# Performance work log

Hardware: AMD Instinct MI355X
Metric: run time of the kernel (lower is better)

Reference implementation:

```python
import jax, jax.numpy as jnp
import numpy as np

HIDDEN = 1024
HEADS = 16
HEAD = HIDDEN // HEADS
EXPAND = 4096
EPS = 1e-5


def layer_norm(x, g, b):
    mu = jnp.mean(x, axis=-1, keepdims=True)
    var = jnp.mean((x - mu) ** 2, axis=-1, keepdims=True)
    return (x - mu) * jax.lax.rsqrt(var + EPS) * g + b


def setup_inputs() -> dict:
    key = jax.random.key(0)
    ks = jax.random.split(key, 12)
    s = 0.02
    return {
        "x": jax.random.normal(ks[0], (4, 2048, HIDDEN), dtype=jnp.float32),
        "Wqkv": jax.random.normal(ks[1], (HIDDEN, 3 * HIDDEN), dtype=jnp.float32) * s,
        "bqkv": jnp.zeros((3 * HIDDEN,), jnp.float32),
        "Wproj": jax.random.normal(ks[2], (HIDDEN, HIDDEN), dtype=jnp.float32) * s,
        "bproj": jnp.zeros((HIDDEN,), jnp.float32),
        "W1": jax.random.normal(ks[3], (HIDDEN, EXPAND), dtype=jnp.float32) * s,
        "b1": jnp.zeros((EXPAND,), jnp.float32),
        "W2": jax.random.normal(ks[4], (EXPAND, HIDDEN), dtype=jnp.float32) * s,
        "b2": jnp.zeros((HIDDEN,), jnp.float32),
        "g1": jnp.ones((HIDDEN,), jnp.float32),
        "be1": jnp.zeros((HIDDEN,), jnp.float32),
        "g2": jnp.ones((HIDDEN,), jnp.float32),
        "be2": jnp.zeros((HIDDEN,), jnp.float32),
    }


def attention(x, Wqkv, bqkv, Wproj, bproj):
    B, L, _ = x.shape
    qkv = (x @ Wqkv + bqkv).reshape(B, L, 3, HEADS, HEAD)
    q, k, v = [qkv[:, :, i].transpose(0, 2, 1, 3) for i in range(3)]  # [B,H,L,D]
    attn = jnp.einsum("bnld,bnkd->bnlk", q, k) / np.sqrt(HEAD).astype(np.float32)
    attn = jax.nn.softmax(attn, axis=-1)
    o = jnp.einsum("bnlk,bnkd->bnld", attn, v)
    o = o.transpose(0, 2, 1, 3).reshape(B, L, HIDDEN)
    return o @ Wproj + bproj


def reference(x, Wqkv, bqkv, Wproj, bproj, W1, b1, W2, b2, g1, be1, g2, be2):
    # post-norm transformer block (pre_norm=False), dropout=0 (eval)
    h = layer_norm(x + attention(x, Wqkv, bqkv, Wproj, bproj), g1, be1)
    ff = jax.nn.gelu(h @ W1 + b1, approximate=False) @ W2 + b2
    return layer_norm(h + ff, g2, be2)
```

## Files before the change

kernel.cpp:

```cpp
#include <hip/hip_runtime.h>
#include <hip/hip_bf16.h>
#include <math.h>


typedef __bf16 bf16_t;
typedef __bf16 bf16x8 __attribute__((ext_vector_type(8)));
typedef __bf16 bf16x4 __attribute__((ext_vector_type(4)));
typedef float f32x4 __attribute__((ext_vector_type(4)));
typedef float f32x16 __attribute__((ext_vector_type(16)));

#define HID   1024
#define NHEAD 16
#define HD    64
#define EXPD  4096
#define LSEQ  2048
#define BATCH 4
#define MROWS (BATCH * LSEQ)

#if __has_builtin(__builtin_amdgcn_exp2f)
#define EXP2F __builtin_amdgcn_exp2f
#else
#define EXP2F exp2f
#endif

__device__ __forceinline__ void gld_lds16(const bf16_t* g, bf16_t* l) {
  __builtin_amdgcn_global_load_lds(
      (const __attribute__((address_space(1))) void*)g,
      (__attribute__((address_space(3))) void*)l, 16, 0, 0);
}

__device__ __forceinline__ void vmwait(int n) {
  if (n == 8)      asm volatile("s_waitcnt vmcnt(8)" ::: "memory");
  else if (n == 4) asm volatile("s_waitcnt vmcnt(4)" ::: "memory");
  else if (n == 3) asm volatile("s_waitcnt vmcnt(3)" ::: "memory");
  else if (n == 0) asm volatile("s_waitcnt vmcnt(0)" ::: "memory");
}

__device__ __forceinline__ void block_bar() {
  asm volatile("" ::: "memory");
  __builtin_amdgcn_s_barrier();
  asm volatile("" ::: "memory");
}

__device__ __forceinline__ void swap32(unsigned& a, unsigned& b) {
#if __has_builtin(__builtin_amdgcn_permlane32_swap)
  auto r = __builtin_amdgcn_permlane32_swap(a, b, false, false);
  a = r[0]; b = r[1];
#else
  bool hiL = ((threadIdx.x & 63) >= 32);
  unsigned pa = (unsigned)__shfl_xor((int)a, 32, 64);
  unsigned pb = (unsigned)__shfl_xor((int)b, 32, 64);
  unsigned na = hiL ? pb : a;
  unsigned nb = hiL ? b : pa;
  a = na; b = nb;
#endif
}

__device__ __forceinline__ unsigned pk_bf16(float lo, float hi) {
  bf16_t l = (bf16_t)lo, h = (bf16_t)hi;
  unsigned short ul, uh;
  __builtin_memcpy(&ul, &l, 2);
  __builtin_memcpy(&uh, &h, 2);
  return (unsigned)ul | ((unsigned)uh << 16);
}

__device__ __forceinline__ float gelu_t(float v) {
  float u = v * (0.7978845608028654f + 0.0356774081f * v * v);
  float e = EXP2F(u * 2.885390082f);
  float th = (e - 1.f) / (e + 1.f);
  return 0.5f * v * (1.f + th);
}

__global__ __launch_bounds__(256) void cvt_bf16(const float* __restrict__ in,
                                                bf16_t* __restrict__ out, int n4) {
  int i = blockIdx.x * 256 + threadIdx.x;
  if (i >= n4) return;
  float4 v = ((const float4*)in)[i];
  bf16x4 o;
  o[0] = (bf16_t)v.x; o[1] = (bf16_t)v.y; o[2] = (bf16_t)v.z; o[3] = (bf16_t)v.w;
  ((bf16x4*)out)[i] = o;
}

__global__ __launch_bounds__(256) void transpose_cvt(const float* __restrict__ W,
                                                     bf16_t* __restrict__ Wt,
                                                     int K, int N) {
  __shared__ float tile[32][33];
  int n0 = blockIdx.x * 32, k0 = blockIdx.y * 32;
  int tx = threadIdx.x & 31, ty = threadIdx.x >> 5;
#pragma unroll
  for (int i = 0; i < 32; i += 8)
    tile[ty + i][tx] = W[(size_t)(k0 + ty + i) * N + n0 + tx];
  __syncthreads();
#pragma unroll
  for (int i = 0; i < 32; i += 8)
    Wt[(size_t)(n0 + ty + i) * K + k0 + tx] = (bf16_t)tile[tx][ty + i];
}

template <int BM, int BN, int NTHR>
__global__ __launch_bounds__(NTHR, (NTHR == 512 ? 4 : 3))
void gemm_k(const bf16_t* __restrict__ A,
            const bf16_t* __restrict__ Bt,
            const float* __restrict__ bias,
            void* __restrict__ C,
            float* __restrict__ C2,
            bf16_t* __restrict__ vTo,
            int M, int N, int K, int mode) {
  constexpr int WC = (NTHR / 64) / 2;
  constexpr int AL = BM * 4 / NTHR;
  constexpr int BL = BN * 4 / NTHR;
  constexpr int LOADS = AL + BL;
  constexpr int RSTEP = NTHR >> 2;
  __shared__ bf16_t smem[3 * BM * 32 + 3 * BN * 32];
  bf16_t* As = smem;
  bf16_t* Bs = smem + 3 * BM * 32;

  const int nbx = gridDim.x;
  int p = blockIdx.y * nbx + blockIdx.x;
  const int GM = 8;
  int group = p / (GM * nbx);
  int idx = p - group * (GM * nbx);
  const int by = group * GM + (idx & (GM - 1));
  const int bx = idx >> 3;
  const int n0 = bx * BN, m0 = by * BM;

  const int zz = blockIdx.z;
  const int kLen = K / (int)gridDim.z;
  const int kOff = zz * kLen;

  const int t = threadIdx.x;
  const int lane = t & 63, w = t >> 6;
  const int wr = w / WC, wc = w % WC;
  const int quad = lane >> 4, l16 = lane & 15;

  f32x4 acc[4][4];
#pragma unroll
  for (int i = 0; i < 4; ++i)
#pragma unroll
    for (int j = 0; j < 4; ++j) acc[i][j] = (f32x4){0.f, 0.f, 0.f, 0.f};

  const int r0 = t >> 2;
  const unsigned ksw = (((unsigned)t & 3u) ^ ((unsigned)(r0 >> 1) & 3u)) * 8u;
  const unsigned offR0 = (unsigned)r0 * (unsigned)K + ksw;

  const bf16_t* aB = A + (size_t)m0 * K + kOff;
  const bf16_t* bB = Bt + (size_t)n0 * K + kOff;

  unsigned aoff[4], boff[4];
#pragma unroll
  for (int i = 0; i < 4; ++i) {
    int row = wr * 64 + 16 * i + l16;
    aoff[i] = (unsigned)(row * 32 + (quad ^ ((row >> 1) & 3)) * 8);
  }
#pragma unroll
  for (int j = 0; j < 4; ++j) {
    int row = wc * 64 + 16 * j + l16;
    boff[j] = (unsigned)(row * 32 + (quad ^ ((row >> 1) & 3)) * 8);
  }

  auto stage = [&](int slot, int kk) {
    bf16_t* Asl = As + slot * (BM * 32);
    bf16_t* Bsl = Bs + slot * (BN * 32);
    const bf16_t* aS = aB + kk;
    const bf16_t* bS = bB + kk;
#pragma unroll
    for (int a = 0; a < AL; ++a)
      gld_lds16(aS + offR0 + (size_t)a * RSTEP * K, Asl + (t + a * NTHR) * 8);
#pragma unroll
    for (int b = 0; b < BL; ++b)
      gld_lds16(bS + offR0 + (size_t)b * RSTEP * K, Bsl + (t + b * NTHR) * 8);
  };

  const int NT = kLen >> 5;

  stage(0, 0);
  stage(1, 32);
  vmwait(LOADS);
  block_bar();

  int cs = 0;
  for (int kt = 0; kt < NT; ++kt) {
    if (kt < NT - 2) {
      int ss = cs == 0 ? 2 : cs - 1;
      stage(ss, (kt + 2) * 32);
    }
    const bf16_t* Asl = As + cs * (BM * 32);
    const bf16_t* Bsl = Bs + cs * (BN * 32);
    bf16x8 af[4], bfr[4];
#pragma unroll
    for (int i = 0; i < 4; ++i) af[i] = *(const bf16x8*)(Asl + aoff[i]);
#pragma unroll
    for (int j = 0; j < 4; ++j) bfr[j] = *(const bf16x8*)(Bsl + boff[j]);
    __builtin_amdgcn_s_setprio(1);
#pragma unroll
    for (int i = 0; i < 4; ++i)
#pragma unroll
      for (int j = 0; j < 4; ++j)
        acc[i][j] = __builtin_amdgcn_mfma_f32_16x16x32_bf16(af[i], bfr[j], acc[i][j], 0, 0, 0);
    __builtin_amdgcn_s_setprio(0);
    if (kt < NT - 2)      vmwait(LOADS);
    else if (kt == NT - 2) vmwait(0);
    if (kt < NT - 1) block_bar();
    cs = cs == 2 ? 0 : cs + 1;
  }

  if constexpr (BN == 256) {
    if (vTo != nullptr && n0 >= 2048) {
      const int bb = m0 >> 11;
      const int l0b = m0 & 2047;
      block_bar();
      bf16_t* T = smem;
#pragma unroll
      for (int i = 0; i < 4; ++i) {
        int rl = wr * 64 + 16 * i + quad * 4;
#pragma unroll
        for (int j = 0; j < 4; ++j) {
          int c = wc * 64 + 16 * j + l16;
          float bv = bias[n0 + c];
          bf16x4 pk;
#pragma unroll
          for (int r = 0; r < 4; ++r) pk[r] = (bf16_t)(acc[i][j][r] + bv);
          *(bf16x4*)(T + c * 132 + rl) = pk;
        }
      }
      block_bar();
      const int vbase = n0 - 2048;
#pragma unroll
      for (int s = 0; s < 4096 / NTHR; ++s) {
        int id = t + s * NTHR;
        int c = id >> 4, ch = id & 15;
        int hh = (vbase + c) >> 6, dd = (vbase + c) & 63;
        bf16x8 v8 = *(const bf16x8*)(T + c * 132 + ch * 8);
        *(bf16x8*)(vTo + ((size_t)((bb * 16 + hh) * 64 + dd)) * 2048 + l0b + ch * 8) = v8;
      }
      return;
    }
  }

#pragma unroll
  for (int i = 0; i < 4; ++i) {
    int rowb = m0 + wr * 64 + 16 * i + quad * 4;
#pragma unroll
    for (int j = 0; j < 4; ++j) {
      int col = n0 + wc * 64 + 16 * j + l16;
      float bv = (zz == 0) ? bias[col] : 0.f;
#pragma unroll
      for (int r = 0; r < 4; ++r) {
        float v = acc[i][j][r] + bv;
        size_t idx = (size_t)(rowb + r) * N + col;
        if (zz != 0) {
          C2[idx] = v;
        } else if (mode == 0) {
          ((bf16_t*)C)[idx] = (bf16_t)v;
        } else if (mode == 1) {
          ((bf16_t*)C)[idx] = (bf16_t)gelu_t(v);
        } else {
          ((float*)C)[idx] = v;
        }
      }
    }
  }
}

__global__ __launch_bounds__(512, 2)
void gemm_8x(const bf16_t* __restrict__ A,
             const bf16_t* __restrict__ Bt,
             const float* __restrict__ bias,
             bf16_t* __restrict__ C,
             int M, int N, int K) {
  __shared__ bf16_t smem[65536];
  const int nbx = gridDim.x;
  int p = blockIdx.y * nbx + blockIdx.x;
  const int GM = 8;
  int group = p / (GM * nbx);
  int idx = p - group * (GM * nbx);
  const int by = group * GM + (idx & (GM - 1));
  const int bx = idx >> 3;
  const int n0 = bx * 256, m0 = by * 256;

  const int t = threadIdx.x;
  const int lane = t & 63, w = t >> 6;
  const int wr = w >> 2, wc = w & 3;
  const int quad = lane >> 4, l16 = lane & 15;

  f32x4 acc[8][4];
#pragma unroll
  for (int i = 0; i < 8; ++i)
#pragma unroll
    for (int j = 0; j < 4; ++j) acc[i][j] = (f32x4){0.f, 0.f, 0.f, 0.f};

  const int r0 = t >> 2;
  const unsigned ksw = (((unsigned)t & 3u) ^ ((unsigned)(r0 >> 1) & 3u)) * 8u;
  const unsigned offR = (unsigned)r0 * (unsigned)K + ksw;

  const bf16_t* aB = A + (size_t)m0 * K;
  const bf16_t* bB = Bt + (size_t)n0 * K;

  unsigned aoff[8], boff[4];
#pragma unroll
  for (int i = 0; i < 8; ++i) {
    int row = wr * 128 + 16 * i + l16;
    aoff[i] = (unsigned)(row * 32 + (quad ^ ((row >> 1) & 3)) * 8);
  }
#pragma unroll
  for (int j = 0; j < 4; ++j) {
    int row = wc * 64 + 16 * j + l16;
    boff[j] = (unsigned)(16384 + row * 32 + (quad ^ ((row >> 1) & 3)) * 8);
  }

  auto stageChunk = [&](const bf16_t* src, int kk, int regionElem) {
    bf16_t* d = smem + regionElem;
    gld_lds16(src + kk + offR, d + t * 8);
    gld_lds16(src + kk + offR + (size_t)128 * K, d + t * 8 + 4096);
  };

  const int NT = K >> 6;

  stageChunk(aB, 0, 0);
  stageChunk(bB, 0, 16384);
  stageChunk(aB, 32, 8192);
  stageChunk(bB, 32, 24576);
  vmwait(4);
  block_bar();

  for (int kt = 0; kt < NT; ++kt) {
    const int sb = (kt & 1) * 32768;
    const int ss = ((kt + 1) & 1) * 32768;
    const int ktk = (kt + 1) * 64;
    const bool st = (kt + 1 < NT);
    bf16x8 af[8], b0, b1;
#pragma unroll
    for (int i = 0; i < 8; ++i) af[i] = *(const bf16x8*)(smem + sb + aoff[i]);
    b0 = *(const bf16x8*)(smem + sb + boff[0]);
    b1 = *(const bf16x8*)(smem + sb + boff[1]);
    if (st) stageChunk(aB, ktk, ss);
    __builtin_amdgcn_s_setprio(1);
#pragma unroll
    for (int i = 0; i < 8; ++i) {
      acc[i][0] = __builtin_amdgcn_mfma_f32_16x16x32_bf16(af[i], b0, acc[i][0], 0, 0, 0);
      acc[i][1] = __builtin_amdgcn_mfma_f32_16x16x32_bf16(af[i], b1, acc[i][1], 0, 0, 0);
    }
    __builtin_amdgcn_s_setprio(0);
    b0 = *(const bf16x8*)(smem + sb + boff[2]);
    b1 = *(const bf16x8*)(smem + sb + boff[3]);
    if (st) stageChunk(bB, ktk, ss + 16384);
    __builtin_amdgcn_s_setprio(1);
#pragma unroll
    for (int i = 0; i < 8; ++i) {
      acc[i][2] = __builtin_amdgcn_mfma_f32_16x16x32_bf16(af[i], b0, acc[i][2], 0, 0, 0);
      acc[i][3] = __builtin_amdgcn_mfma_f32_16x16x32_bf16(af[i], b1, acc[i][3], 0, 0, 0);
    }
    __builtin_amdgcn_s_setprio(0);
    if (st) vmwait(4); else vmwait(0);
    block_bar();
#pragma unroll
    for (int i = 0; i < 8; ++i) af[i] = *(const bf16x8*)(smem + sb + 8192 + aoff[i]);
    b0 = *(const bf16x8*)(smem + sb + 8192 + boff[0]);
    b1 = *(const bf16x8*)(smem + sb + 8192 + boff[1]);
    if (st) stageChunk(aB, ktk + 32, ss + 8192);
    __builtin_amdgcn_s_setprio(1);
#pragma unroll
    for (int i = 0; i < 8; ++i) {
      acc[i][0] = __builtin_amdgcn_mfma_f32_16x16x32_bf16(af[i], b0, acc[i][0], 0, 0, 0);
      acc[i][1] = __builtin_amdgcn_mfma_f32_16x16x32_bf16(af[i], b1, acc[i][1], 0, 0, 0);
    }
    __builtin_amdgcn_s_setprio(0);
    b0 = *(const bf16x8*)(smem + sb + 8192 + boff[2]);
    b1 = *(const bf16x8*)(smem + sb + 8192 + boff[3]);
    if (st) stageChunk(bB, ktk + 32, ss + 24576);
    __builtin_amdgcn_s_setprio(1);
#pragma unroll
    for (int i = 0; i < 8; ++i) {
      acc[i][2] = __builtin_amdgcn_mfma_f32_16x16x32_bf16(af[i], b0, acc[i][2], 0, 0, 0);
      acc[i][3] = __builtin_amdgcn_mfma_f32_16x16x32_bf16(af[i], b1, acc[i][3], 0, 0, 0);
    }
    __builtin_amdgcn_s_setprio(0);
    if (st) {
      vmwait(4);
      block_bar();
    }
  }

#pragma unroll
  for (int i = 0; i < 8; ++i) {
    int rowb = m0 + wr * 128 + 16 * i + quad * 4;
#pragma unroll
    for (int j = 0; j < 4; ++j) {
      int col = n0 + wc * 64 + 16 * j + l16;
      float bv = bias[col];
#pragma unroll
      for (int r = 0; r < 4; ++r) {
        float v = acc[i][j][r] + bv;
        C[(size_t)(rowb + r) * N + col] = (bf16_t)gelu_t(v);
      }
    }
  }
}

__global__ __launch_bounds__(256, 2) void attn_kernel(const bf16_t* __restrict__ qkv,
                                                      const bf16_t* __restrict__ vT,
                                                      bf16_t* __restrict__ ob) {
  __shared__ bf16_t smem[5 * 128 * 64];
  bf16_t* Qs = smem + 32768;
  const int qt = blockIdx.x, h = blockIdx.y, b = blockIdx.z;
  const int t = threadIdx.x, lane = t & 63, w = t >> 6;
  const int l32 = lane & 31, hi = lane >> 5;
  const size_t RS = 3 * HID;
  const int bh = b * NHEAD + h;

  const bf16_t* qbase = qkv + ((size_t)(b * LSEQ + qt * 128)) * RS + h * HD;
  const bf16_t* kbase = qkv + ((size_t)b * LSEQ) * RS + HID + h * HD;
  const bf16_t* vtbase = vT + (size_t)bh * HD * LSEQ;

#pragma unroll
  for (int s = 0; s < 4; ++s) {
    int l = t + s * 256;
    int r = l >> 3, c8 = l & 7;
    gld_lds16(qbase + (size_t)r * RS + ((c8 ^ (r & 7)) * 8), Qs + l * 8);
  }
  __syncthreads();

  const float sc = 0.18033688011112042f;
  bf16x8 bq[4];
  {
    int qrow = 32 * w + l32;
#pragma unroll
    for (int c = 0; c < 4; ++c) {
      int y = 2 * c + hi;
      bf16x8 q8 = *(const bf16x8*)(Qs + qrow * 64 + ((y ^ (qrow & 7)) * 8));
#pragma unroll
      for (int e = 0; e < 8; ++e) q8[e] = (bf16_t)((float)q8[e] * sc);
      bq[c] = q8;
    }
  }

  auto stageKV = [&](int slot, int kt) {
    bf16_t* Ks = smem + slot * 16384;
    bf16_t* Vts = Ks + 8192;
#pragma unroll
    for (int s = 0; s < 4; ++s) {
      int l = t + s * 256;
      int r = l >> 3, c8 = l & 7;
      gld_lds16(kbase + (size_t)(kt * 128 + r) * RS + ((c8 ^ (r & 7)) * 8), Ks + l * 8);
      int rv = l >> 4, c16 = l & 15;
      gld_lds16(vtbase + (size_t)rv * LSEQ + kt * 128 + ((c16 ^ (rv & 7)) * 8), Vts + l * 8);
    }
  };

  f32x16 accO[2];
#pragma unroll
  for (int dt = 0; dt < 2; ++dt)
#pragma unroll
    for (int e = 0; e < 16; ++e) accO[dt][e] = 0.f;
  float l_acc = 0.f;

  constexpr int NT = LSEQ / 128;
  stageKV(0, 0);

  for (int kt = 0; kt < NT; ++kt) {
    const int cs = kt & 1;
    if (kt + 1 < NT) {
      stageKV(1 - cs, kt + 1);
      vmwait(8);
    } else {
      vmwait(0);
    }
    block_bar();
    const bf16_t* Ks = smem + cs * 16384;
    const bf16_t* Vts = Ks + 8192;

#pragma unroll
    for (int kt2 = 0; kt2 < 2; ++kt2) {
      f32x16 s0, s1;
#pragma unroll
      for (int e = 0; e < 16; ++e) { s0[e] = 0.f; s1[e] = 0.f; }
      __builtin_amdgcn_s_setprio(1);
#pragma unroll
      for (int c = 0; c < 4; ++c) {
        int y = 2 * c + hi;
        int r0 = (2 * kt2 + 0) * 32 + l32;
        bf16x8 a0 = *(const bf16x8*)(Ks + r0 * 64 + ((y ^ (r0 & 7)) * 8));
        s0 = __builtin_amdgcn_mfma_f32_32x32x16_bf16(a0, bq[c], s0, 0, 0, 0);
        int r1 = (2 * kt2 + 1) * 32 + l32;
        bf16x8 a1 = *(const bf16x8*)(Ks + r1 * 64 + ((y ^ (r1 & 7)) * 8));
        s1 = __builtin_amdgcn_mfma_f32_32x32x16_bf16(a1, bq[c], s1, 0, 0, 0);
      }
      __builtin_amdgcn_s_setprio(0);

      unsigned pf[2][2][4];
#pragma unroll
      for (int tile = 0; tile < 2; ++tile) {
        f32x16& sv = tile ? s1 : s0;
        float p[16];
#pragma unroll
        for (int e = 0; e < 16; ++e) { p[e] = EXP2F(sv[e]); l_acc += p[e]; }
        unsigned lo[4], hi_[4];
#pragma unroll
        for (int g = 0; g < 4; ++g) {
          lo[g] = pk_bf16(p[4 * g + 0], p[4 * g + 1]);
          hi_[g] = pk_bf16(p[4 * g + 2], p[4 * g + 3]);
        }
#pragma unroll
        for (int c2 = 0; c2 < 2; ++c2) {
          unsigned aL = lo[2 * c2], bL = lo[2 * c2 + 1];
          swap32(aL, bL);
          pf[tile][c2][0] = aL; pf[tile][c2][2] = bL;
          unsigned aH = hi_[2 * c2], bH = hi_[2 * c2 + 1];
          swap32(aH, bH);
          pf[tile][c2][1] = aH; pf[tile][c2][3] = bH;
        }
      }

      __builtin_amdgcn_s_setprio(1);
#pragma unroll
      for (int dt = 0; dt < 2; ++dt)
#pragma unroll
        for (int tile = 0; tile < 2; ++tile)
#pragma unroll
          for (int c2 = 0; c2 < 2; ++c2) {
            int ktile = 2 * kt2 + tile;
            int c8v = ktile * 4 + c2 * 2 + hi;
            int rv = dt * 32 + l32;
            bf16x8 av = *(const bf16x8*)(Vts + rv * 128 + ((c8v ^ (rv & 7)) * 8));
            union { unsigned u[4]; bf16x8 v; } bp;
            bp.u[0] = pf[tile][c2][0]; bp.u[1] = pf[tile][c2][1];
            bp.u[2] = pf[tile][c2][2]; bp.u[3] = pf[tile][c2][3];
            accO[dt] = __builtin_amdgcn_mfma_f32_32x32x16_bf16(av, bp.v, accO[dt], 0, 0, 0);
          }
      __builtin_amdgcn_s_setprio(0);
    }
    block_bar();
  }

  l_acc += __shfl_xor(l_acc, 32, 64);
  float inv = 1.f / l_acc;

  bf16_t* Osh = smem;
  {
    int q = 32 * w + l32;
#pragma unroll
    for (int dt = 0; dt < 2; ++dt)
#pragma unroll
      for (int e = 0; e < 16; ++e) {
        int d = dt * 32 + (e & 3) + 8 * (e >> 2) + 4 * hi;
        Osh[q * 68 + d] = (bf16_t)(accO[dt][e] * inv);
      }
  }
  __syncthreads();
#pragma unroll
  for (int s = 0; s < 4; ++s) {
    int l = t + s * 256;
    int r = l >> 3, c8 = l & 7;
    bf16x8 v = *(const bf16x8*)(Osh + r * 68 + c8 * 8);
    *(bf16x8*)(ob + ((size_t)(b * LSEQ + qt * 128 + r)) * HID + h * HD + c8 * 8) = v;
  }
}

__global__ __launch_bounds__(256) void resid_ln(const float* __restrict__ X,
                                                const float* __restrict__ Y,
                                                const float* __restrict__ Y2,
                                                const float* __restrict__ g,
                                                const float* __restrict__ be,
                                                float* __restrict__ outf,
                                                bf16_t* __restrict__ outb) {
  const int row = blockIdx.x;
  const int t = threadIdx.x;
  float4 a = ((const float4*)X)[(size_t)row * 256 + t];
  float4 bvec = ((const float4*)Y)[(size_t)row * 256 + t];
  float4 cvec = {0.f, 0.f, 0.f, 0.f};
  if (Y2) cvec = ((const float4*)Y2)[(size_t)row * 256 + t];
  float v0 = a.x + bvec.x + cvec.x, v1 = a.y + bvec.y + cvec.y;
  float v2 = a.z + bvec.z + cvec.z, v3 = a.w + bvec.w + cvec.w;
  float s = v0 + v1 + v2 + v3;
  float s2 = v0 * v0 + v1 * v1 + v2 * v2 + v3 * v3;
#pragma unroll
  for (int msk = 1; msk < 64; msk <<= 1) {
    s += __shfl_xor(s, msk, 64);
    s2 += __shfl_xor(s2, msk, 64);
  }
  __shared__ float red[8];
  int w = t >> 6;
  if ((t & 63) == 0) { red[w] = s; red[w + 4] = s2; }
  __syncthreads();
  s = red[0] + red[1] + red[2] + red[3];
  s2 = red[4] + red[5] + red[6] + red[7];
  float mu = s * (1.f / 1024.f);
  float var = s2 * (1.f / 1024.f) - mu * mu;
  float rstd = rsqrtf(var + 1e-5f);
  float4 gg = ((const float4*)g)[t];
  float4 bb = ((const float4*)be)[t];
  float o0 = (v0 - mu) * rstd * gg.x + bb.x;
  float o1 = (v1 - mu) * rstd * gg.y + bb.y;
  float o2 = (v2 - mu) * rstd * gg.z + bb.z;
  float o3 = (v3 - mu) * rstd * gg.w + bb.w;
  float4 o = {o0, o1, o2, o3};
  ((float4*)outf)[(size_t)row * 256 + t] = o;
  if (outb) {
    bf16x4 ob4;
    ob4[0] = (bf16_t)o0; ob4[1] = (bf16_t)o1; ob4[2] = (bf16_t)o2; ob4[3] = (bf16_t)o3;
    ((bf16x4*)outb)[(size_t)row * 256 + t] = ob4;
  }
}

extern "C" void kernel_launch(void* const* d_in, const int* in_sizes, int n_in,
                              void* d_out, int out_size, void* d_ws, size_t ws_size,
                              hipStream_t stream) {
  const float* x     = (const float*)d_in[0];
  const float* Wqkv  = (const float*)d_in[1];
  const float* bqkv  = (const float*)d_in[2];
  const float* Wproj = (const float*)d_in[3];
  const float* bproj = (const float*)d_in[4];
  const float* W1    = (const float*)d_in[5];
  const float* b1    = (const float*)d_in[6];
  const float* W2    = (const float*)d_in[7];
  const float* b2    = (const float*)d_in[8];
  const float* g1    = (const float*)d_in[9];
  const float* be1   = (const float*)d_in[10];
  const float* g2    = (const float*)d_in[11];
  const float* be2   = (const float*)d_in[12];
  float* out = (float*)d_out;

  char* ws = (char*)d_ws;
  bf16_t* w2T    = (bf16_t*)(ws);
  float*  h      = (float*) (ws + ((size_t)8 << 20));
  float*  a_f2   = (float*) (ws + ((size_t)40 << 20));
  bf16_t* qkv_ff = (bf16_t*)(ws + ((size_t)72 << 20));
  char*   E      = ws + ((size_t)136 << 20);
  bf16_t* wqkvT  = (bf16_t*)(E);
  bf16_t* wprojT = (bf16_t*)(E + ((size_t)6 << 20));
  bf16_t* w1T    = (bf16_t*)(E + ((size_t)8 << 20));
  char*   xb_ob  = E + ((size_t)16 << 20);
  bf16_t* hb     = (bf16_t*)(E + ((size_t)32 << 20));
  float*  f2b    = (float*)E;

  bf16_t* xb    = (bf16_t*)xb_ob;
  bf16_t* ob    = (bf16_t*)xb_ob;
  bf16_t* qkvb  = qkv_ff;
  bf16_t* ff1b  = qkv_ff;
  float*  attnf = a_f2;
  float*  ff2f  = a_f2;
  bf16_t* vTg   = hb;

  dim3 blk(256);
  dim3 blk512(512);
  transpose_cvt<<<dim3(3072 / 32, 1024 / 32), blk, 0, stream>>>(Wqkv, wqkvT, 1024, 3072);
  transpose_cvt<<<dim3(1024 / 32, 1024 / 32), blk, 0, stream>>>(Wproj, wprojT, 1024, 1024);
  transpose_cvt<<<dim3(4096 / 32, 1024 / 32), blk, 0, stream>>>(W1, w1T, 1024, 4096);
  transpose_cvt<<<dim3(1024 / 32, 4096 / 32), blk, 0, stream>>>(W2, w2T, 4096, 1024);
  cvt_bf16<<<MROWS * HID / 4 / 256, blk, 0, stream>>>(x, xb, MROWS * HID / 4);

  gemm_k<128, 256, 512><<<dim3(3072 / 256, MROWS / 128), blk512, 0, stream>>>(
      xb, wqkvT, bqkv, qkvb, nullptr, vTg, MROWS, 3072, 1024, 0);
  attn_kernel<<<dim3(LSEQ / 128, NHEAD, BATCH), blk, 0, stream>>>(qkvb, vTg, ob);
  gemm_k<128, 256, 512><<<dim3(1024 / 256, MROWS / 128, 2), blk512, 0, stream>>>(
      ob, wprojT, bproj, attnf, h, nullptr, MROWS, 1024, 1024, 2);
  resid_ln<<<MROWS, blk, 0, stream>>>(x, attnf, h, g1, be1, h, hb);
  gemm_8x<<<dim3(4096 / 256, MROWS / 256), blk512, 0, stream>>>(
      hb, w1T, b1, ff1b, MROWS, 4096, 1024);
  gemm_k<128, 256, 512><<<dim3(1024 / 256, MROWS / 128, 2), blk512, 0, stream>>>(
      ff1b, w2T, b2, ff2f, f2b, nullptr, MROWS, 1024, 4096, 2);
  resid_ln<<<MROWS, blk, 0, stream>>>(h, ff2f, f2b, g2, be2, out, (bf16_t*)nullptr);
}
```

Measured before the change: 527.7 us.

## Halve attention KV tile to raise occupancy and compute row sums via MFMA

Shrinks the attention K/V staging tile from 128 to 64 keys, which cuts LDS use from 80KB to 48KB and raises the launch bound to 3 blocks per CU. The softmax denominator is now accumulated with an extra MFMA against a ones vector instead of scalar adds and a cross-lane shuffle, so the VALU work moves onto the matrix units. The trade-off is twice as many barrier/stage iterations and four extra MFMAs per tile. The row sum is also built from bf16-rounded probabilities, which slightly changes the numerics.

```diff
diff --git a/kernel.cpp b/kernel.cpp
--- a/kernel.cpp
+++ b/kernel.cpp
@@ -396,11 +396,11 @@
   }
 }
 
-__global__ __launch_bounds__(256, 2) void attn_kernel(const bf16_t* __restrict__ qkv,
+__global__ __launch_bounds__(256, 3) void attn_kernel(const bf16_t* __restrict__ qkv,
                                                       const bf16_t* __restrict__ vT,
                                                       bf16_t* __restrict__ ob) {
-  __shared__ bf16_t smem[5 * 128 * 64];
-  bf16_t* Qs = smem + 32768;
+  __shared__ bf16_t smem[24576];
+  bf16_t* Qs = smem + 16384;
   const int qt = blockIdx.x, h = blockIdx.y, b = blockIdx.z;
   const int t = threadIdx.x, lane = t & 63, w = t >> 6;
   const int l32 = lane & 31, hi = lane >> 5;
@@ -433,106 +433,114 @@
     }
   }
 
+  bf16x8 ones8;
+#pragma unroll
+  for (int e = 0; e < 8; ++e) ones8[e] = (bf16_t)1.0f;
+
   auto stageKV = [&](int slot, int kt) {
-    bf16_t* Ks = smem + slot * 16384;
-    bf16_t* Vts = Ks + 8192;
-#pragma unroll
-    for (int s = 0; s < 4; ++s) {
+    bf16_t* Ks = smem + slot * 8192;
+    bf16_t* Vts = Ks + 4096;
+#pragma unroll
+    for (int s = 0; s < 2; ++s) {
       int l = t + s * 256;
       int r = l >> 3, c8 = l & 7;
-      gld_lds16(kbase + (size_t)(kt * 128 + r) * RS + ((c8 ^ (r & 7)) * 8), Ks + l * 8);
-      int rv = l >> 4, c16 = l & 15;
-      gld_lds16(vtbase + (size_t)rv * LSEQ + kt * 128 + ((c16 ^ (rv & 7)) * 8), Vts + l * 8);
+      gld_lds16(kbase + (size_t)(kt * 64 + r) * RS + ((c8 ^ (r & 7)) * 8), Ks + l * 8);
+      gld_lds16(vtbase + (size_t)r * LSEQ + kt * 64 + ((c8 ^ (r & 7)) * 8), Vts + l * 8);
     }
   };
 
-  f32x16 accO[2];
+  f32x16 accO[2], accS;
 #pragma unroll
   for (int dt = 0; dt < 2; ++dt)
 #pragma unroll
     for (int e = 0; e < 16; ++e) accO[dt][e] = 0.f;
-  float l_acc = 0.f;
-
-  constexpr int NT = LSEQ / 128;
+#pragma unroll
+  for (int e = 0; e < 16; ++e) accS[e] = 0.f;
+
+  constexpr int NT = LSEQ / 64;
   stageKV(0, 0);
 
   for (int kt = 0; kt < NT; ++kt) {
     const int cs = kt & 1;
     if (kt + 1 < NT) {
       stageKV(1 - cs, kt + 1);
-      vmwait(8);
+      vmwait(4);
     } else {
       vmwait(0);
     }
     block_bar();
-    const bf16_t* Ks = smem + cs * 16384;
-    const bf16_t* Vts = Ks + 8192;
-
-#pragma unroll
-    for (int kt2 = 0; kt2 < 2; ++kt2) {
-      f32x16 s0, s1;
-#pragma unroll
-      for (int e = 0; e < 16; ++e) { s0[e] = 0.f; s1[e] = 0.f; }
-      __builtin_amdgcn_s_setprio(1);
-#pragma unroll
-      for (int c = 0; c < 4; ++c) {
-        int y = 2 * c + hi;
-        int r0 = (2 * kt2 + 0) * 32 + l32;
-        bf16x8 a0 = *(const bf16x8*)(Ks + r0 * 64 + ((y ^ (r0 & 7)) * 8));
-        s0 = __builtin_amdgcn_mfma_f32_32x32x16_bf16(a0, bq[c], s0, 0, 0, 0);
-        int r1 = (2 * kt2 + 1) * 32 + l32;
-        bf16x8 a1 = *(const bf16x8*)(Ks + r1 * 64 + ((y ^ (r1 & 7)) * 8));
-        s1 = __builtin_amdgcn_mfma_f32_32x32x16_bf16(a1, bq[c], s1, 0, 0, 0);
-      }
-      __builtin_amdgcn_s_setprio(0);
-
-      unsigned pf[2][2][4];
-#pragma unroll
-      for (int tile = 0; tile < 2; ++tile) {
-        f32x16& sv = tile ? s1 : s0;
-        float p[16];
-#pragma unroll
-        for (int e = 0; e < 16; ++e) { p[e] = EXP2F(sv[e]); l_acc += p[e]; }
-        unsigned lo[4], hi_[4];
-#pragma unroll
-        for (int g = 0; g < 4; ++g) {
-          lo[g] = pk_bf16(p[4 * g + 0], p[4 * g + 1]);
-          hi_[g] = pk_bf16(p[4 * g + 2], p[4 * g + 3]);
+    const bf16_t* Ks = smem + cs * 8192;
+    const bf16_t* Vts = Ks + 4096;
+
+    f32x16 s0, s1;
+#pragma unroll
+    for (int e = 0; e < 16; ++e) { s0[e] = 0.f; s1[e] = 0.f; }
+    __builtin_amdgcn_s_setprio(1);
+#pragma unroll
+    for (int c = 0; c < 4; ++c) {
+      int y = 2 * c + hi;
+      int r0 = l32;
+      bf16x8 a0 = *(const bf16x8*)(Ks + r0 * 64 + ((y ^ (r0 & 7)) * 8));
+      s0 = __builtin_amdgcn_mfma_f32_32x32x16_bf16(a0, bq[c], s0, 0, 0, 0);
+      int r1 = 32 + l32;
+      bf16x8 a1 = *(const bf16x8*)(Ks + r1 * 64 + ((y ^ (r1 & 7)) * 8));
+      s1 = __builtin_amdgcn_mfma_f32_32x32x16_bf16(a1, bq[c], s1, 0, 0, 0);
+    }
+    __builtin_amdgcn_s_setprio(0);
+
+    unsigned pf[2][2][4];
+#pragma unroll
+    for (int stile = 0; stile < 2; ++stile) {
+      f32x16& sv = stile ? s1 : s0;
+      float p[16];
+#pragma unroll
+      for (int e = 0; e < 16; ++e) p[e] = EXP2F(sv[e]);
+      unsigned lo[4], hi_[4];
+#pragma unroll
+      for (int g = 0; g < 4; ++g) {
+        lo[g] = pk_bf16(p[4 * g + 0], p[4 * g + 1]);
+        hi_[g] = pk_bf16(p[4 * g + 2], p[4 * g + 3]);
+      }
+#pragma unroll
+      for (int c2 = 0; c2 < 2; ++c2) {
+        unsigned aL = lo[2 * c2], bL = lo[2 * c2 + 1];
+        swap32(aL, bL);
+        pf[stile][c2][0] = aL; pf[stile][c2][2] = bL;
+        unsigned aH = hi_[2 * c2], bH = hi_[2 * c2 + 1];
+        swap32(aH, bH);
+        pf[stile][c2][1] = aH; pf[stile][c2][3] = bH;
+      }
+    }
+
+    __builtin_amdgcn_s_setprio(1);
+#pragma unroll
+    for (int dt = 0; dt < 2; ++dt)
+#pragma unroll
+      for (int stile = 0; stile < 2; ++stile)
+#pragma unroll
+        for (int c2 = 0; c2 < 2; ++c2) {
+          int c8v = stile * 4 + c2 * 2 + hi;
+          int rv = dt * 32 + l32;
+          bf16x8 av = *(const bf16x8*)(Vts + rv * 64 + ((c8v ^ (rv & 7)) * 8));
+          union { unsigned u[4]; bf16x8 v; } bp;
+          bp.u[0] = pf[stile][c2][0]; bp.u[1] = pf[stile][c2][1];
+          bp.u[2] = pf[stile][c2][2]; bp.u[3] = pf[stile][c2][3];
+          accO[dt] = __builtin_amdgcn_mfma_f32_32x32x16_bf16(av, bp.v, accO[dt], 0, 0, 0);
         }
 #pragma unroll
-        for (int c2 = 0; c2 < 2; ++c2) {
-          unsigned aL = lo[2 * c2], bL = lo[2 * c2 + 1];
-          swap32(aL, bL);
-          pf[tile][c2][0] = aL; pf[tile][c2][2] = bL;
-          unsigned aH = hi_[2 * c2], bH = hi_[2 * c2 + 1];
-          swap32(aH, bH);
-          pf[tile][c2][1] = aH; pf[tile][c2][3] = bH;
-        }
-      }
-
-      __builtin_amdgcn_s_setprio(1);
-#pragma unroll
-      for (int dt = 0; dt < 2; ++dt)
-#pragma unroll
-        for (int tile = 0; tile < 2; ++tile)
-#pragma unroll
-          for (int c2 = 0; c2 < 2; ++c2) {
-            int ktile = 2 * kt2 + tile;
-            int c8v = ktile * 4 + c2 * 2 + hi;
-            int rv = dt * 32 + l32;
-            bf16x8 av = *(const bf16x8*)(Vts + rv * 128 + ((c8v ^ (rv & 7)) * 8));
-            union { unsigned u[4]; bf16x8 v; } bp;
-            bp.u[0] = pf[tile][c2][0]; bp.u[1] = pf[tile][c2][1];
-            bp.u[2] = pf[tile][c2][2]; bp.u[3] = pf[tile][c2][3];
-            accO[dt] = __builtin_amdgcn_mfma_f32_32x32x16_bf16(av, bp.v, accO[dt], 0, 0, 0);
-          }
-      __builtin_amdgcn_s_setprio(0);
-    }
+    for (int stile = 0; stile < 2; ++stile)
+#pragma unroll
+      for (int c2 = 0; c2 < 2; ++c2) {
+        union { unsigned u[4]; bf16x8 v; } bp;
+        bp.u[0] = pf[stile][c2][0]; bp.u[1] = pf[stile][c2][1];
+        bp.u[2] = pf[stile][c2][2]; bp.u[3] = pf[stile][c2][3];
+        accS = __builtin_amdgcn_mfma_f32_32x32x16_bf16(ones8, bp.v, accS, 0, 0, 0);
+      }
+    __builtin_amdgcn_s_setprio(0);
     block_bar();
   }
 
-  l_acc += __shfl_xor(l_acc, 32, 64);
-  float inv = 1.f / l_acc;
+  float inv = 1.f / accS[0];
 
   bf16_t* Osh = smem;
   {
```

After: 532.0 us. About the same (+0.8%).
